# Optimization experiments

Hardware: AMD Instinct MI355X
Metric: run time of the kernel (lower is better)

## Reference

```python
import jax, jax.numpy as jnp
import numpy as np

D_MODEL = 256
N_HEADS = 8


def setup_inputs() -> dict:
    key = jax.random.key(0)
    ks = jax.random.split(key, 12)
    B, S, d, H = 4, 1024, D_MODEL, N_HEADS
    s = 0.02
    return {
        "Q": jax.random.normal(ks[0], (B, S, d), jnp.float32),
        "K": jax.random.normal(ks[1], (B, S, d), jnp.float32),
        "V": jax.random.normal(ks[2], (B, S, d), jnp.float32),
        "Wq": jax.random.normal(ks[3], (d, d * H), jnp.float32) * s,
        "bq": jnp.zeros((d * H,), jnp.float32),
        "Wk": jax.random.normal(ks[4], (d, d * H), jnp.float32) * s,
        "bk": jnp.zeros((d * H,), jnp.float32),
        "Wv": jax.random.normal(ks[5], (d, d * H), jnp.float32) * s,
        "bv": jnp.zeros((d * H,), jnp.float32),
        "Wo": jax.random.normal(ks[6], (H * d, d), jnp.float32) * s,
        "bo": jnp.zeros((d,), jnp.float32),
    }


def reference(Q, K, V, Wq, bq, Wk, bk, Wv, bv, Wo, bo):
    B, S, d = Q.shape
    H = N_HEADS
    # projections: [B,S,d] -> [B,S,H*d] -> [B,H,S,d] (head_dim == d_model here)
    q = (Q @ Wq + bq).reshape(B, S, H, d).transpose(0, 2, 1, 3)
    k = (K @ Wk + bk).reshape(B, S, H, d).transpose(0, 2, 1, 3)
    v = (V @ Wv + bv).reshape(B, S, H, d).transpose(0, 2, 1, 3)
    scores = jnp.einsum("bhqd,bhkd->bhqk", q, k) / jnp.sqrt(jnp.float32(d))
    attn = jax.nn.softmax(scores, axis=-1)
    out = jnp.einsum("bhqk,bhkd->bhqd", attn, v)  # [B,H,S,d]
    out = out.transpose(0, 2, 1, 3).reshape(B, S, H * d)
    return out @ Wo + bo
```

## Files before the change

kernel.cpp:

```cpp
#include <hip/hip_runtime.h>
#include <stdint.h>

#define NB 4
#define SEQ 1024
#define DM 256
#define NH 8

typedef __attribute__((ext_vector_type(8))) short bf8;
typedef __attribute__((ext_vector_type(4))) float f4;

__device__ __forceinline__ unsigned short f2bf(float f) {
  union { float f; uint32_t u; } c; c.f = f;
  uint32_t u = c.u;
  return (unsigned short)((u + 0x7FFFu + ((u >> 16) & 1u)) >> 16);
}

__device__ __forceinline__ void gl_lds16(const unsigned short* g, short* l) {
  __builtin_amdgcn_global_load_lds(
      (const __attribute__((address_space(1))) unsigned int*)g,
      (__attribute__((address_space(3))) unsigned int*)l, 16, 0, 0);
}


__global__ __launch_bounds__(256) void prep_kernel(
    const float* __restrict__ Wq, const float* __restrict__ Wk,
    const float* __restrict__ Wv, const float* __restrict__ Wo,
    const float* __restrict__ Q, const float* __restrict__ K,
    const float* __restrict__ V,
    unsigned short* __restrict__ Wt3, unsigned short* __restrict__ WoT,
    unsigned short* __restrict__ Xbf) {
  const int z = blockIdx.y;
  const int tid = threadIdx.x;
  if (z >= 4) {
    const float* src = (z == 4) ? Q : (z == 5) ? K : V;
    const size_t off = (size_t)blockIdx.x * 1024 + tid * 4;
    const float4 v = *(const float4*)(src + off);
    short4 s;
    s.x = (short)f2bf(v.x); s.y = (short)f2bf(v.y);
    s.z = (short)f2bf(v.z); s.w = (short)f2bf(v.w);
    *(short4*)(Xbf + (size_t)(z - 4) * 4096 * 256 + off) = s;
    return;
  }
  if (blockIdx.x >= 512) return;
  const float* in;
  unsigned short* out;
  int R, C, bx, by;
  if (z < 3) {
    in = (z == 0) ? Wq : (z == 1) ? Wk : Wv;
    out = Wt3 + (size_t)z * 2048 * 256;
    R = 256; C = 2048; bx = blockIdx.x & 63; by = blockIdx.x >> 6;
  } else {
    in = Wo; out = WoT;
    R = 2048; C = 256; bx = blockIdx.x & 7; by = blockIdx.x >> 3;
  }
  __shared__ float t[32][33];
  const int c0 = bx * 32, r0 = by * 32;
  const int tx = tid & 31, ty = tid >> 5;
#pragma unroll
  for (int i = 0; i < 4; i++) {
    int r = r0 + ty + i * 8;
    t[ty + i * 8][tx] = in[(size_t)r * C + c0 + tx];
  }
  __syncthreads();
#pragma unroll
  for (int i = 0; i < 4; i++) {
    int c = c0 + ty + i * 8;
    out[(size_t)c * R + r0 + tx] = f2bf(t[tx][ty + i * 8]);
  }
}

__global__ __launch_bounds__(256) void proj_kernel(
    const unsigned short* __restrict__ Xbf, const unsigned short* __restrict__ Wt3,
    const float* __restrict__ bq, const float* __restrict__ bk, const float* __restrict__ bv,
    unsigned short* __restrict__ q_frag, unsigned short* __restrict__ k_frag,
    unsigned short* __restrict__ v_frag) {
  const int z = blockIdx.z;
  const unsigned short* X = Xbf + (size_t)z * 4096 * 256;
  const unsigned short* Wt = Wt3 + (size_t)z * 2048 * 256;
  const float* bias = (z == 0) ? bq : (z == 1) ? bk : bv;

  __shared__ short a_lds[128 * 32];
  __shared__ short b_lds[128 * 32];

  const int tid = threadIdx.x;
  const int wid = tid >> 6, lane = tid & 63;
  const int quad = lane >> 4, l16 = lane & 15;
  const int wm = wid >> 1, wn = wid & 1;
  const int m0 = blockIdx.x * 128, n0 = blockIdx.y * 128;

  f4 acc[4][4];
  const f4 z4 = {0.f, 0.f, 0.f, 0.f};
#pragma unroll
  for (int i = 0; i < 4; i++)
#pragma unroll
    for (int j = 0; j < 4; j++) acc[i][j] = z4;

  const int srow = lane >> 2;
  const int schunk = lane & 3;
  const int cxor = quad ^ (l16 & 3);

  for (int ko = 0; ko < 8; ko++) {
    const int k0 = ko * 32;
#pragma unroll
    for (int j = 0; j < 2; j++) {
      const int i = wid * 2 + j;
      const int row = i * 16 + srow;
      const int sc = (schunk ^ (row & 3)) * 8;
      gl_lds16(X + (size_t)(m0 + row) * DM + k0 + sc, a_lds + i * 512);
      gl_lds16(Wt + (size_t)(n0 + row) * DM + k0 + sc, b_lds + i * 512);
    }
    __syncthreads();
    bf8 af[4], bfv[4];
#pragma unroll
    for (int mi = 0; mi < 4; mi++)
      af[mi] = *(const bf8*)(a_lds + (wm * 64 + mi * 16 + l16) * 32 + cxor * 8);
#pragma unroll
    for (int ni = 0; ni < 4; ni++)
      bfv[ni] = *(const bf8*)(b_lds + (wn * 64 + ni * 16 + l16) * 32 + cxor * 8);
    if (z < 2) {
#pragma unroll
      for (int ni = 0; ni < 4; ni++)
#pragma unroll
        for (int mi = 0; mi < 4; mi++)
          acc[ni][mi] = __builtin_amdgcn_mfma_f32_16x16x32_bf16(bfv[ni], af[mi], acc[ni][mi], 0, 0, 0);
    } else {
#pragma unroll
      for (int mi = 0; mi < 4; mi++)
#pragma unroll
        for (int ni = 0; ni < 4; ni++)
          acc[mi][ni] = __builtin_amdgcn_mfma_f32_16x16x32_bf16(af[mi], bfv[ni], acc[mi][ni], 0, 0, 0);
    }
    __syncthreads();
  }

  if (z < 2) {
    const float scale = (z == 0) ? 0.0901684400f : 1.0f;
    unsigned short* dst = (z == 0) ? q_frag : k_frag;
#pragma unroll
    for (int ni = 0; ni < 4; ni++) {
      const int nb = n0 + wn * 64 + ni * 16 + quad * 4;
      const float4 b4 = *(const float4*)(bias + nb);
      const int h = nb >> 8, dd = nb & 255;
      const int dq = (dd >> 3) & 3, jh = dd & 7;
#pragma unroll
      for (int mi = 0; mi < 4; mi++) {
        const int tok = m0 + wm * 64 + mi * 16 + l16;
        const int b = tok >> 10, sr = tok & 1023;
        const size_t idx = ((size_t)(b * NH + h) * 64 + (sr >> 4)) * 4096 +
                           (size_t)(dd >> 5) * 512 + ((sr & 15) + 16 * dq) * 8 + jh;
        short4 s4;
        s4.x = (short)f2bf((acc[ni][mi][0] + b4.x) * scale);
        s4.y = (short)f2bf((acc[ni][mi][1] + b4.y) * scale);
        s4.z = (short)f2bf((acc[ni][mi][2] + b4.z) * scale);
        s4.w = (short)f2bf((acc[ni][mi][3] + b4.w) * scale);
        *(short4*)(dst + idx) = s4;
      }
    }
  } else {
#pragma unroll
    for (int ni = 0; ni < 4; ni++) {
      const int n = n0 + wn * 64 + ni * 16 + l16;
      const float bsv = bias[n];
      const int h = n >> 8, d = n & 255;
#pragma unroll
      for (int mi = 0; mi < 4; mi++) {
        const int m = m0 + wm * 64 + mi * 16 + quad * 4;
        const int b = m >> 10, sr = m & 1023;
        const size_t idx = ((size_t)(b * NH + h) * 16 + (d >> 4)) * 16384 +
                           (size_t)(sr >> 5) * 512 +
                           ((d & 15) + 16 * ((sr >> 3) & 3)) * 8 + (sr & 7);
        short4 s4;
        s4.x = (short)f2bf(acc[mi][ni][0] + bsv);
        s4.y = (short)f2bf(acc[mi][ni][1] + bsv);
        s4.z = (short)f2bf(acc[mi][ni][2] + bsv);
        s4.w = (short)f2bf(acc[mi][ni][3] + bsv);
        *(short4*)(v_frag + idx) = s4;
      }
    }
  }
}

__global__ __launch_bounds__(256) void attn_kernel(
    const unsigned short* __restrict__ q_frag, const unsigned short* __restrict__ k_frag,
    const unsigned short* __restrict__ v_frag, unsigned short* __restrict__ o_ws) {
  __shared__ short k_lds[2][8192];
  __shared__ short p_lds[2][64][40];
  __shared__ float l_sh[64];

  const int tid = threadIdx.x;
  const int wid = tid >> 6, lane = tid & 63;
  const int quad = lane >> 4, l16 = lane & 15;
  const int blk = blockIdx.x;
  const int g = blk & 7;
  const int qt = (blk >> 3) & 15;
  const int bh = g + 8 * (blk >> 7);
  const size_t fbase = (size_t)bh * 262144;

  bf8 qf[8];
  {
    const unsigned short* qp = q_frag + fbase + (size_t)(qt * 4 + wid) * 4096 + lane * 8;
#pragma unroll
    for (int kc = 0; kc < 8; kc++) qf[kc] = *(const bf8*)(qp + kc * 512);
  }

  const f4 z4 = {0.f, 0.f, 0.f, 0.f};
  f4 Oacc[4][4];
#pragma unroll
  for (int i = 0; i < 4; i++)
#pragma unroll
    for (int j = 0; j < 4; j++) Oacc[i][j] = z4;
  float lpart[4] = {0.f, 0.f, 0.f, 0.f};

  const unsigned short* kdma_src = k_frag + fbase + (size_t)wid * 2048 + lane * 8;
#pragma unroll
  for (int jj = 0; jj < 4; jj++)
    gl_lds16(kdma_src + jj * 512, &k_lds[0][wid * 2048 + jj * 512]);
  __syncthreads();

  bf8 vpre0[4], vpre1[4];
  const unsigned short* vbase_p = v_frag + fbase + (size_t)(wid * 4) * 16384 + lane * 8;

#define ATTN_STEP(T, CUR, PRV, VCUR, VPRV)                                     \
  {                                                                            \
    const int t_ = (T);                                                        \
    _Pragma("unroll")                                                          \
    for (int mi = 0; mi < 4; mi++)                                             \
      VCUR[mi] = *(const bf8*)(vbase_p + (size_t)mi * 16384 + (size_t)t_ * 512); \
    f4 Sacc[2];                                                                \
    Sacc[0] = z4; Sacc[1] = z4;                                                \
    _Pragma("unroll")                                                          \
    for (int kc = 0; kc < 8; kc++) {                                           \
      const bf8 aq = qf[kc];                                                   \
      _Pragma("unroll")                                                        \
      for (int ni = 0; ni < 2; ni++) {                                         \
        const bf8 kb = *(const bf8*)(&k_lds[CUR][(ni * 8 + kc) * 512 + lane * 8]); \
        Sacc[ni] = __builtin_amdgcn_mfma_f32_16x16x32_bf16(aq, kb, Sacc[ni], 0, 0, 0); \
      }                                                                        \
    }                                                                          \
    if (t_ < 31) {                                                             \
      _Pragma("unroll")                                                        \
      for (int jj = 0; jj < 4; jj++)                                           \
        gl_lds16(kdma_src + (size_t)(t_ + 1) * 8192 + jj * 512,                \
                 &k_lds[PRV][wid * 2048 + jj * 512]);                          \
    }                                                                          \
    if (t_ > 0) {                                                              \
      bf8 pb[4];                                                               \
      _Pragma("unroll")                                                        \
      for (int nq = 0; nq < 4; nq++)                                           \
        pb[nq] = *(const bf8*)(&p_lds[PRV][nq * 16 + l16][quad * 8]);          \
      _Pragma("unroll")                                                        \
      for (int mi = 0; mi < 4; mi++)                                           \
        _Pragma("unroll")                                                      \
        for (int nq = 0; nq < 4; nq++)                                         \
          Oacc[mi][nq] = __builtin_amdgcn_mfma_f32_16x16x32_bf16(VPRV[mi], pb[nq], Oacc[mi][nq], 0, 0, 0); \
    }                                                                          \
    _Pragma("unroll")                                                          \
    for (int reg = 0; reg < 4; reg++) {                                        \
      const int qrow = wid * 16 + quad * 4 + reg;                              \
      float s = 0.f;                                                           \
      _Pragma("unroll")                                                        \
      for (int ni = 0; ni < 2; ni++) {                                         \
        const float p = exp2f(Sacc[ni][reg]);                                  \
        s += p;                                                                \
        union { float f; uint32_t u; } c;                                      \
        c.f = p;                                                               \
        p_lds[CUR][qrow][ni * 16 + l16] = (short)((c.u + 0x8000u) >> 16);      \
      }                                                                        \
      lpart[reg] += s;                                                         \
    }                                                                          \
    __syncthreads();                                                           \
  }

  for (int tt = 0; tt < 16; tt++) {
    ATTN_STEP(tt * 2, 0, 1, vpre0, vpre1)
    ATTN_STEP(tt * 2 + 1, 1, 0, vpre1, vpre0)
  }
#undef ATTN_STEP

  {
    bf8 pb[4];
#pragma unroll
    for (int nq = 0; nq < 4; nq++)
      pb[nq] = *(const bf8*)(&p_lds[1][nq * 16 + l16][quad * 8]);
#pragma unroll
    for (int mi = 0; mi < 4; mi++)
#pragma unroll
      for (int nq = 0; nq < 4; nq++)
        Oacc[mi][nq] = __builtin_amdgcn_mfma_f32_16x16x32_bf16(vpre1[mi], pb[nq], Oacc[mi][nq], 0, 0, 0);
  }

#pragma unroll
  for (int reg = 0; reg < 4; reg++) {
    float v = lpart[reg];
    v += __shfl_xor(v, 1, 64);
    v += __shfl_xor(v, 2, 64);
    v += __shfl_xor(v, 4, 64);
    v += __shfl_xor(v, 8, 64);
    if (l16 == 0) l_sh[wid * 16 + quad * 4 + reg] = v;
  }
  __syncthreads();

  const int b = bh >> 3, h = bh & 7;
#pragma unroll
  for (int nq = 0; nq < 4; nq++) {
    const int q = nq * 16 + l16;
    const float inv = 1.f / l_sh[q];
    const size_t base = ((size_t)b * SEQ + qt * 64 + q) * (NH * DM) + h * DM + wid * 64;
#pragma unroll
    for (int mi = 0; mi < 4; mi++) {
      short4 s4;
      s4.x = (short)f2bf(Oacc[mi][nq][0] * inv);
      s4.y = (short)f2bf(Oacc[mi][nq][1] * inv);
      s4.z = (short)f2bf(Oacc[mi][nq][2] * inv);
      s4.w = (short)f2bf(Oacc[mi][nq][3] * inv);
      *(short4*)(o_ws + base + mi * 16 + quad * 4) = s4;
    }
  }
}

__global__ __launch_bounds__(256) void outproj_kernel(
    const unsigned short* __restrict__ o_ws, const unsigned short* __restrict__ WoT,
    const float* __restrict__ bo, float* __restrict__ out) {
  __shared__ short a_lds[32][136];
  __shared__ short b_lds[64][136];

  const int tid = threadIdx.x;
  const int wid = tid >> 6, lane = tid & 63;
  const int quad = lane >> 4, l16 = lane & 15;
  const int wm = wid & 1, wn = wid >> 1;
  const int m0 = blockIdx.x * 32, n0 = blockIdx.y * 64;

  const f4 z4 = {0.f, 0.f, 0.f, 0.f};
  f4 acc[2];
#pragma unroll
  for (int i = 0; i < 2; i++) acc[i] = z4;

  const int ch = tid & 15, row = tid >> 4;
  for (int ko = 0; ko < 16; ko++) {
    const int k0 = ko * 128;
#pragma unroll
    for (int rb = 0; rb < 2; rb++) {
      int r = row + rb * 16;
      *(bf8*)(&a_lds[r][ch * 8]) = *(const bf8*)(o_ws + (size_t)(m0 + r) * 2048 + k0 + ch * 8);
    }
#pragma unroll
    for (int rb = 0; rb < 4; rb++) {
      int r = row + rb * 16;
      *(bf8*)(&b_lds[r][ch * 8]) = *(const bf8*)(WoT + (size_t)(n0 + r) * 2048 + k0 + ch * 8);
    }
    __syncthreads();
#pragma unroll
    for (int kc = 0; kc < 4; kc++) {
      const bf8 af = *(const bf8*)(&a_lds[wm * 16 + l16][kc * 32 + quad * 8]);
      bf8 bfv[2];
#pragma unroll
      for (int ni = 0; ni < 2; ni++)
        bfv[ni] = *(const bf8*)(&b_lds[wn * 32 + ni * 16 + l16][kc * 32 + quad * 8]);
#pragma unroll
      for (int ni = 0; ni < 2; ni++)
        acc[ni] = __builtin_amdgcn_mfma_f32_16x16x32_bf16(af, bfv[ni], acc[ni], 0, 0, 0);
    }
    __syncthreads();
  }
#pragma unroll
  for (int ni = 0; ni < 2; ni++) {
    const int n = n0 + wn * 32 + ni * 16 + l16;
    const float bv = bo[n];
#pragma unroll
    for (int reg = 0; reg < 4; reg++) {
      const int m = m0 + wm * 16 + quad * 4 + reg;
      out[(size_t)m * DM + n] = acc[ni][reg] + bv;
    }
  }
}

extern "C" void kernel_launch(void* const* d_in, const int* in_sizes, int n_in,
                              void* d_out, int out_size, void* d_ws, size_t ws_size,
                              hipStream_t stream) {
  const float* Q  = (const float*)d_in[0];
  const float* K  = (const float*)d_in[1];
  const float* V  = (const float*)d_in[2];
  const float* Wq = (const float*)d_in[3];
  const float* bq = (const float*)d_in[4];
  const float* Wk = (const float*)d_in[5];
  const float* bk = (const float*)d_in[6];
  const float* Wv = (const float*)d_in[7];
  const float* bv = (const float*)d_in[8];
  const float* Wo = (const float*)d_in[9];
  const float* bo = (const float*)d_in[10];
  float* out = (float*)d_out;

  char* ws = (char*)d_ws;
  const size_t QS = (size_t)NB * NH * SEQ * DM * 2;
  unsigned short* q_frag = (unsigned short*)(ws);
  unsigned short* k_frag = (unsigned short*)(ws + QS);
  unsigned short* v_frag = (unsigned short*)(ws + 2 * QS);
  unsigned short* o_ws   = (unsigned short*)(ws + 3 * QS);
  const size_t WT = (size_t)2048 * 256 * 2;
  unsigned short* Wt3 = (unsigned short*)(ws + 4 * QS);
  unsigned short* WoT = (unsigned short*)(ws + 4 * QS + 3 * WT);
  unsigned short* Xbf = o_ws;

  prep_kernel<<<dim3(1024, 7), 256, 0, stream>>>(Wq, Wk, Wv, Wo, Q, K, V,
                                                 Wt3, WoT, Xbf);
  proj_kernel<<<dim3(32, 16, 3), 256, 0, stream>>>(Xbf, Wt3, bq, bk, bv,
                                                   q_frag, k_frag, v_frag);
  attn_kernel<<<512, 256, 0, stream>>>(q_frag, k_frag, v_frag, o_ws);
  outproj_kernel<<<dim3(128, 4), 256, 0, stream>>>(o_ws, WoT, bo, out);
}
```

Measured before the change: 168.8 us.

## Process 64-key tiles per step with 2x2 wave split in attention kernel

New measurement: 171.0 us. Within noise of the previous version (+1.3%).

```diff
diff --git a/kernel.cpp b/kernel.cpp
--- a/kernel.cpp
+++ b/kernel.cpp
@@ -180,27 +180,37 @@
   }
 }
 
-__global__ __launch_bounds__(256) void attn_kernel(
+__global__ __launch_bounds__(256, 2) void attn_kernel(
     const unsigned short* __restrict__ q_frag, const unsigned short* __restrict__ k_frag,
     const unsigned short* __restrict__ v_frag, unsigned short* __restrict__ o_ws) {
-  __shared__ short k_lds[2][8192];
-  __shared__ short p_lds[2][64][40];
-  __shared__ float l_sh[64];
+  __shared__ short k_lds[3 * 8192];
+  __shared__ short p_lds[2][2][64][40];
+  __shared__ float l_sh[2][64];
 
   const int tid = threadIdx.x;
   const int wid = tid >> 6, lane = tid & 63;
   const int quad = lane >> 4, l16 = lane & 15;
+  const int wq = wid >> 1, wk = wid & 1;
   const int blk = blockIdx.x;
   const int g = blk & 7;
   const int qt = (blk >> 3) & 15;
   const int bh = g + 8 * (blk >> 7);
   const size_t fbase = (size_t)bh * 262144;
 
-  bf8 qf[8];
-  {
-    const unsigned short* qp = q_frag + fbase + (size_t)(qt * 4 + wid) * 4096 + lane * 8;
-#pragma unroll
-    for (int kc = 0; kc < 8; kc++) qf[kc] = *(const bf8*)(qp + kc * 512);
+  const unsigned short* ksrc = k_frag + fbase + (size_t)wid * 2048 + lane * 8;
+#pragma unroll
+  for (int jj = 0; jj < 4; jj++) {
+    gl_lds16(ksrc + jj * 512, &k_lds[wid * 2048 + jj * 512]);
+    gl_lds16(ksrc + 8192 + jj * 512, &k_lds[2 * 8192 + wid * 2048 + jj * 512]);
+  }
+
+  bf8 qf[2][8];
+#pragma unroll
+  for (int qi = 0; qi < 2; qi++) {
+    const unsigned short* qp =
+        q_frag + fbase + (size_t)(qt * 4 + wq * 2 + qi) * 4096 + lane * 8;
+#pragma unroll
+    for (int c = 0; c < 8; c++) qf[qi][c] = *(const bf8*)(qp + c * 512);
   }
 
   const f4 z4 = {0.f, 0.f, 0.f, 0.f};
@@ -209,102 +219,121 @@
   for (int i = 0; i < 4; i++)
 #pragma unroll
     for (int j = 0; j < 4; j++) Oacc[i][j] = z4;
-  float lpart[4] = {0.f, 0.f, 0.f, 0.f};
-
-  const unsigned short* kdma_src = k_frag + fbase + (size_t)wid * 2048 + lane * 8;
-#pragma unroll
-  for (int jj = 0; jj < 4; jj++)
-    gl_lds16(kdma_src + jj * 512, &k_lds[0][wid * 2048 + jj * 512]);
+  float lpart[2][4] = {{0.f, 0.f, 0.f, 0.f}, {0.f, 0.f, 0.f, 0.f}};
+
   __syncthreads();
 
-  bf8 vpre0[4], vpre1[4];
-  const unsigned short* vbase_p = v_frag + fbase + (size_t)(wid * 4) * 16384 + lane * 8;
-
-#define ATTN_STEP(T, CUR, PRV, VCUR, VPRV)                                     \
-  {                                                                            \
-    const int t_ = (T);                                                        \
-    _Pragma("unroll")                                                          \
-    for (int mi = 0; mi < 4; mi++)                                             \
-      VCUR[mi] = *(const bf8*)(vbase_p + (size_t)mi * 16384 + (size_t)t_ * 512); \
-    f4 Sacc[2];                                                                \
-    Sacc[0] = z4; Sacc[1] = z4;                                                \
-    _Pragma("unroll")                                                          \
-    for (int kc = 0; kc < 8; kc++) {                                           \
-      const bf8 aq = qf[kc];                                                   \
-      _Pragma("unroll")                                                        \
-      for (int ni = 0; ni < 2; ni++) {                                         \
-        const bf8 kb = *(const bf8*)(&k_lds[CUR][(ni * 8 + kc) * 512 + lane * 8]); \
-        Sacc[ni] = __builtin_amdgcn_mfma_f32_16x16x32_bf16(aq, kb, Sacc[ni], 0, 0, 0); \
-      }                                                                        \
-    }                                                                          \
-    if (t_ < 31) {                                                             \
-      _Pragma("unroll")                                                        \
-      for (int jj = 0; jj < 4; jj++)                                           \
-        gl_lds16(kdma_src + (size_t)(t_ + 1) * 8192 + jj * 512,                \
-                 &k_lds[PRV][wid * 2048 + jj * 512]);                          \
-    }                                                                          \
-    if (t_ > 0) {                                                              \
-      bf8 pb[4];                                                               \
-      _Pragma("unroll")                                                        \
-      for (int nq = 0; nq < 4; nq++)                                           \
-        pb[nq] = *(const bf8*)(&p_lds[PRV][nq * 16 + l16][quad * 8]);          \
-      _Pragma("unroll")                                                        \
-      for (int mi = 0; mi < 4; mi++)                                           \
-        _Pragma("unroll")                                                      \
-        for (int nq = 0; nq < 4; nq++)                                         \
-          Oacc[mi][nq] = __builtin_amdgcn_mfma_f32_16x16x32_bf16(VPRV[mi], pb[nq], Oacc[mi][nq], 0, 0, 0); \
-    }                                                                          \
-    _Pragma("unroll")                                                          \
-    for (int reg = 0; reg < 4; reg++) {                                        \
-      const int qrow = wid * 16 + quad * 4 + reg;                              \
-      float s = 0.f;                                                           \
-      _Pragma("unroll")                                                        \
-      for (int ni = 0; ni < 2; ni++) {                                         \
-        const float p = exp2f(Sacc[ni][reg]);                                  \
-        s += p;                                                                \
-        union { float f; uint32_t u; } c;                                      \
-        c.f = p;                                                               \
-        p_lds[CUR][qrow][ni * 16 + l16] = (short)((c.u + 0x8000u) >> 16);      \
-      }                                                                        \
-      lpart[reg] += s;                                                         \
-    }                                                                          \
-    __syncthreads();                                                           \
-  }
-
-  for (int tt = 0; tt < 16; tt++) {
-    ATTN_STEP(tt * 2, 0, 1, vpre0, vpre1)
-    ATTN_STEP(tt * 2 + 1, 1, 0, vpre1, vpre0)
-  }
-#undef ATTN_STEP
+  bf8 vpre[8];
+  const unsigned short* vsrc = v_frag + fbase + (size_t)(wid * 4) * 16384 + lane * 8;
+
+  for (int t = 0; t < 16; t++) {
+    const int cur = t & 1;
+    if (t < 15) {
+      const unsigned short* s0 = ksrc + (size_t)(t + 1) * 16384;
+#pragma unroll
+      for (int jj = 0; jj < 4; jj++)
+        gl_lds16(s0 + jj * 512, &k_lds[(cur ^ 1) * 8192 + wid * 2048 + jj * 512]);
+    }
+    const short* kb_base = &k_lds[(wk ? 2 : cur) * 8192];
+    f4 S00 = z4, S01 = z4, S10 = z4, S11 = z4;
+#pragma unroll
+    for (int c = 0; c < 8; c++) {
+      const bf8 kb0 = *(const bf8*)(kb_base + c * 512 + lane * 8);
+      const bf8 kb1 = *(const bf8*)(kb_base + 4096 + c * 512 + lane * 8);
+      S00 = __builtin_amdgcn_mfma_f32_16x16x32_bf16(qf[0][c], kb0, S00, 0, 0, 0);
+      S01 = __builtin_amdgcn_mfma_f32_16x16x32_bf16(qf[0][c], kb1, S01, 0, 0, 0);
+      S10 = __builtin_amdgcn_mfma_f32_16x16x32_bf16(qf[1][c], kb0, S10, 0, 0, 0);
+      S11 = __builtin_amdgcn_mfma_f32_16x16x32_bf16(qf[1][c], kb1, S11, 0, 0, 0);
+    }
+    __syncthreads();
+    if (t < 15) {
+      const unsigned short* s1 = ksrc + (size_t)(t + 1) * 16384 + 8192;
+#pragma unroll
+      for (int jj = 0; jj < 4; jj++)
+        gl_lds16(s1 + jj * 512, &k_lds[2 * 8192 + wid * 2048 + jj * 512]);
+    }
+    if (t > 0) {
+      const int prv = cur ^ 1;
+#pragma unroll
+      for (int ks = 0; ks < 2; ks++) {
+        bf8 pb[4];
+#pragma unroll
+        for (int nq = 0; nq < 4; nq++)
+          pb[nq] = *(const bf8*)(&p_lds[prv][ks][nq * 16 + l16][quad * 8]);
+#pragma unroll
+        for (int mi = 0; mi < 4; mi++)
+#pragma unroll
+          for (int nq = 0; nq < 4; nq++)
+            Oacc[mi][nq] = __builtin_amdgcn_mfma_f32_16x16x32_bf16(
+                vpre[ks * 4 + mi], pb[nq], Oacc[mi][nq], 0, 0, 0);
+      }
+    }
+#pragma unroll
+    for (int ks = 0; ks < 2; ks++)
+#pragma unroll
+      for (int mi = 0; mi < 4; mi++)
+        vpre[ks * 4 + mi] =
+            *(const bf8*)(vsrc + (size_t)mi * 16384 + (size_t)(2 * t + ks) * 512);
+#pragma unroll
+    for (int reg = 0; reg < 4; reg++) {
+      {
+        const int qrow = wq * 32 + quad * 4 + reg;
+        const float p0 = exp2f(S00[reg]);
+        const float p1 = exp2f(S01[reg]);
+        lpart[0][reg] += p0 + p1;
+        union { float f; uint32_t u; } c0, c1;
+        c0.f = p0; c1.f = p1;
+        p_lds[cur][wk][qrow][l16] = (short)((c0.u + 0x8000u) >> 16);
+        p_lds[cur][wk][qrow][16 + l16] = (short)((c1.u + 0x8000u) >> 16);
+      }
+      {
+        const int qrow = wq * 32 + 16 + quad * 4 + reg;
+        const float p0 = exp2f(S10[reg]);
+        const float p1 = exp2f(S11[reg]);
+        lpart[1][reg] += p0 + p1;
+        union { float f; uint32_t u; } c0, c1;
+        c0.f = p0; c1.f = p1;
+        p_lds[cur][wk][qrow][l16] = (short)((c0.u + 0x8000u) >> 16);
+        p_lds[cur][wk][qrow][16 + l16] = (short)((c1.u + 0x8000u) >> 16);
+      }
+    }
+    __syncthreads();
+  }
 
   {
-    bf8 pb[4];
-#pragma unroll
-    for (int nq = 0; nq < 4; nq++)
-      pb[nq] = *(const bf8*)(&p_lds[1][nq * 16 + l16][quad * 8]);
-#pragma unroll
-    for (int mi = 0; mi < 4; mi++)
+#pragma unroll
+    for (int ks = 0; ks < 2; ks++) {
+      bf8 pb[4];
 #pragma unroll
       for (int nq = 0; nq < 4; nq++)
-        Oacc[mi][nq] = __builtin_amdgcn_mfma_f32_16x16x32_bf16(vpre1[mi], pb[nq], Oacc[mi][nq], 0, 0, 0);
-  }
-
-#pragma unroll
-  for (int reg = 0; reg < 4; reg++) {
-    float v = lpart[reg];
-    v += __shfl_xor(v, 1, 64);
-    v += __shfl_xor(v, 2, 64);
-    v += __shfl_xor(v, 4, 64);
-    v += __shfl_xor(v, 8, 64);
-    if (l16 == 0) l_sh[wid * 16 + quad * 4 + reg] = v;
-  }
+        pb[nq] = *(const bf8*)(&p_lds[1][ks][nq * 16 + l16][quad * 8]);
+#pragma unroll
+      for (int mi = 0; mi < 4; mi++)
+#pragma unroll
+        for (int nq = 0; nq < 4; nq++)
+          Oacc[mi][nq] = __builtin_amdgcn_mfma_f32_16x16x32_bf16(
+              vpre[ks * 4 + mi], pb[nq], Oacc[mi][nq], 0, 0, 0);
+    }
+  }
+
+#pragma unroll
+  for (int qi = 0; qi < 2; qi++)
+#pragma unroll
+    for (int reg = 0; reg < 4; reg++) {
+      float v = lpart[qi][reg];
+      v += __shfl_xor(v, 1, 64);
+      v += __shfl_xor(v, 2, 64);
+      v += __shfl_xor(v, 4, 64);
+      v += __shfl_xor(v, 8, 64);
+      if (l16 == 0) l_sh[wk][wq * 32 + qi * 16 + quad * 4 + reg] = v;
+    }
   __syncthreads();
 
   const int b = bh >> 3, h = bh & 7;
 #pragma unroll
   for (int nq = 0; nq < 4; nq++) {
     const int q = nq * 16 + l16;
-    const float inv = 1.f / l_sh[q];
+    const float inv = 1.f / (l_sh[0][q] + l_sh[1][q]);
     const size_t base = ((size_t)b * SEQ + qt * 64 + q) * (NH * DM) + h * DM + wid * 64;
 #pragma unroll
     for (int mi = 0; mi < 4; mi++) {
```

## Split attention KV range across two blocks and merge partials in output projection

Applied to the files above, without the earlier changes.

Result: slower. 187.1 us (+10.9%).

```diff
diff --git a/kernel.cpp b/kernel.cpp
--- a/kernel.cpp
+++ b/kernel.cpp
@@ -13,6 +13,12 @@
   union { float f; uint32_t u; } c; c.f = f;
   uint32_t u = c.u;
   return (unsigned short)((u + 0x7FFFu + ((u >> 16) & 1u)) >> 16);
+}
+
+__device__ __forceinline__ float bf2f(short s) {
+  union { uint32_t u; float f; } c;
+  c.u = ((uint32_t)(unsigned short)s) << 16;
+  return c.f;
 }
 
 __device__ __forceinline__ void gl_lds16(const unsigned short* g, short* l) {
@@ -180,12 +186,12 @@
   }
 }
 
-__global__ __launch_bounds__(256) void attn_kernel(
+__global__ __launch_bounds__(256, 3) void attn_kernel(
     const unsigned short* __restrict__ q_frag, const unsigned short* __restrict__ k_frag,
-    const unsigned short* __restrict__ v_frag, unsigned short* __restrict__ o_ws) {
+    const unsigned short* __restrict__ v_frag, unsigned short* __restrict__ o_p0,
+    unsigned short* __restrict__ o_p1, float* __restrict__ l_part, const int split) {
   __shared__ short k_lds[2][8192];
   __shared__ short p_lds[2][64][40];
-  __shared__ float l_sh[64];
 
   const int tid = threadIdx.x;
   const int wid = tid >> 6, lane = tid & 63;
@@ -193,7 +199,11 @@
   const int blk = blockIdx.x;
   const int g = blk & 7;
   const int qt = (blk >> 3) & 15;
-  const int bh = g + 8 * (blk >> 7);
+  const int kvh = split ? ((blk >> 7) & 1) : 0;
+  const int bh = g + 8 * (blk >> (split ? 8 : 7));
+  const int t0 = kvh * 16;
+  const int tlast = t0 + (split ? 15 : 31);
+  const int nhalf = split ? 8 : 16;
   const size_t fbase = (size_t)bh * 262144;
 
   bf8 qf[8];
@@ -214,7 +224,7 @@
   const unsigned short* kdma_src = k_frag + fbase + (size_t)wid * 2048 + lane * 8;
 #pragma unroll
   for (int jj = 0; jj < 4; jj++)
-    gl_lds16(kdma_src + jj * 512, &k_lds[0][wid * 2048 + jj * 512]);
+    gl_lds16(kdma_src + (size_t)t0 * 8192 + jj * 512, &k_lds[0][wid * 2048 + jj * 512]);
   __syncthreads();
 
   bf8 vpre0[4], vpre1[4];
@@ -237,13 +247,13 @@
         Sacc[ni] = __builtin_amdgcn_mfma_f32_16x16x32_bf16(aq, kb, Sacc[ni], 0, 0, 0); \
       }                                                                        \
     }                                                                          \
-    if (t_ < 31) {                                                             \
+    if (t_ < tlast) {                                                          \
       _Pragma("unroll")                                                        \
       for (int jj = 0; jj < 4; jj++)                                           \
         gl_lds16(kdma_src + (size_t)(t_ + 1) * 8192 + jj * 512,                \
                  &k_lds[PRV][wid * 2048 + jj * 512]);                          \
     }                                                                          \
-    if (t_ > 0) {                                                              \
+    if (t_ > t0) {                                                             \
       bf8 pb[4];                                                               \
       _Pragma("unroll")                                                        \
       for (int nq = 0; nq < 4; nq++)                                           \
@@ -271,9 +281,9 @@
     __syncthreads();                                                           \
   }
 
-  for (int tt = 0; tt < 16; tt++) {
-    ATTN_STEP(tt * 2, 0, 1, vpre0, vpre1)
-    ATTN_STEP(tt * 2 + 1, 1, 0, vpre1, vpre0)
+  for (int tt = 0; tt < nhalf; tt++) {
+    ATTN_STEP(t0 + tt * 2, 0, 1, vpre0, vpre1)
+    ATTN_STEP(t0 + tt * 2 + 1, 1, 0, vpre1, vpre0)
   }
 #undef ATTN_STEP
 
@@ -296,30 +306,34 @@
     v += __shfl_xor(v, 2, 64);
     v += __shfl_xor(v, 4, 64);
     v += __shfl_xor(v, 8, 64);
-    if (l16 == 0) l_sh[wid * 16 + quad * 4 + reg] = v;
-  }
-  __syncthreads();
-
+    if (l16 == 0) {
+      const size_t lidx = (size_t)bh * 1024 + qt * 64 + wid * 16 + quad * 4 + reg;
+      l_part[(size_t)kvh * 32768 + lidx] = v;
+      if (!split) l_part[32768 + lidx] = v;
+    }
+  }
+
+  unsigned short* op = kvh ? o_p1 : o_p0;
   const int b = bh >> 3, h = bh & 7;
 #pragma unroll
   for (int nq = 0; nq < 4; nq++) {
     const int q = nq * 16 + l16;
-    const float inv = 1.f / l_sh[q];
     const size_t base = ((size_t)b * SEQ + qt * 64 + q) * (NH * DM) + h * DM + wid * 64;
 #pragma unroll
     for (int mi = 0; mi < 4; mi++) {
       short4 s4;
-      s4.x = (short)f2bf(Oacc[mi][nq][0] * inv);
-      s4.y = (short)f2bf(Oacc[mi][nq][1] * inv);
-      s4.z = (short)f2bf(Oacc[mi][nq][2] * inv);
-      s4.w = (short)f2bf(Oacc[mi][nq][3] * inv);
-      *(short4*)(o_ws + base + mi * 16 + quad * 4) = s4;
+      s4.x = (short)f2bf(Oacc[mi][nq][0]);
+      s4.y = (short)f2bf(Oacc[mi][nq][1]);
+      s4.z = (short)f2bf(Oacc[mi][nq][2]);
+      s4.w = (short)f2bf(Oacc[mi][nq][3]);
+      *(short4*)(op + base + mi * 16 + quad * 4) = s4;
     }
   }
 }
 
 __global__ __launch_bounds__(256) void outproj_kernel(
-    const unsigned short* __restrict__ o_ws, const unsigned short* __restrict__ WoT,
+    const unsigned short* __restrict__ o_p0, const unsigned short* __restrict__ o_p1,
+    const float* __restrict__ l_part, const unsigned short* __restrict__ WoT,
     const float* __restrict__ bo, float* __restrict__ out) {
   __shared__ short a_lds[32][136];
   __shared__ short b_lds[64][136];
@@ -338,10 +352,21 @@
   const int ch = tid & 15, row = tid >> 4;
   for (int ko = 0; ko < 16; ko++) {
     const int k0 = ko * 128;
+    const int h = k0 >> 8;
 #pragma unroll
     for (int rb = 0; rb < 2; rb++) {
-      int r = row + rb * 16;
-      *(bf8*)(&a_lds[r][ch * 8]) = *(const bf8*)(o_ws + (size_t)(m0 + r) * 2048 + k0 + ch * 8);
+      const int r = row + rb * 16;
+      const int token = m0 + r;
+      const int b_ = token >> 10, sr = token & 1023;
+      const size_t lidx = (size_t)(b_ * NH + h) * 1024 + sr;
+      const float inv = 1.f / (l_part[lidx] + l_part[32768 + lidx]);
+      const bf8 v0 = *(const bf8*)(o_p0 + (size_t)token * 2048 + k0 + ch * 8);
+      const bf8 v1 = *(const bf8*)(o_p1 + (size_t)token * 2048 + k0 + ch * 8);
+      bf8 s;
+#pragma unroll
+      for (int j = 0; j < 8; j++)
+        s[j] = (short)f2bf((bf2f(v0[j]) + bf2f(v1[j])) * inv);
+      *(bf8*)(&a_lds[r][ch * 8]) = s;
     }
 #pragma unroll
     for (int rb = 0; rb < 4; rb++) {
@@ -392,19 +417,24 @@
 
   char* ws = (char*)d_ws;
   const size_t QS = (size_t)NB * NH * SEQ * DM * 2;
+  const size_t WT = (size_t)2048 * 256 * 2;
   unsigned short* q_frag = (unsigned short*)(ws);
   unsigned short* k_frag = (unsigned short*)(ws + QS);
   unsigned short* v_frag = (unsigned short*)(ws + 2 * QS);
-  unsigned short* o_ws   = (unsigned short*)(ws + 3 * QS);
-  const size_t WT = (size_t)2048 * 256 * 2;
+  unsigned short* o_p0   = (unsigned short*)(ws + 3 * QS);
   unsigned short* Wt3 = (unsigned short*)(ws + 4 * QS);
   unsigned short* WoT = (unsigned short*)(ws + 4 * QS + 3 * WT);
-  unsigned short* Xbf = o_ws;
+  float* l_part = (float*)(ws + 4 * QS);
+  const size_t need_split = 4 * QS + 4 * WT + QS;
+  const int split = (ws_size >= need_split) ? 1 : 0;
+  unsigned short* o_p1 = split ? (unsigned short*)(ws + 4 * QS + 4 * WT) : o_p0;
+  unsigned short* Xbf = o_p0;
 
   prep_kernel<<<dim3(1024, 7), 256, 0, stream>>>(Wq, Wk, Wv, Wo, Q, K, V,
                                                  Wt3, WoT, Xbf);
   proj_kernel<<<dim3(32, 16, 3), 256, 0, stream>>>(Xbf, Wt3, bq, bk, bv,
                                                    q_frag, k_frag, v_frag);
-  attn_kernel<<<512, 256, 0, stream>>>(q_frag, k_frag, v_frag, o_ws);
-  outproj_kernel<<<dim3(128, 4), 256, 0, stream>>>(o_ws, WoT, bo, out);
-}
+  attn_kernel<<<split ? 1024 : 512, 256, 0, stream>>>(q_frag, k_frag, v_frag,
+                                                      o_p0, o_p1, l_part, split);
+  outproj_kernel<<<dim3(128, 4), 256, 0, stream>>>(o_p0, o_p1, l_part, WoT, bo, out);
+}
```
